# Kernel optimization log

Hardware: AMD Instinct MI355X
Metric: run time of the kernel (lower is better)

## Reference

```python
import jax, jax.numpy as jnp
import numpy as np
import math

HEAD_SIZE = 64

def setup_inputs() -> dict:
    key = jax.random.key(0)
    k0, k1, k2, k3 = jax.random.split(key, 4)
    B, T, E, H = 4, 4096, 1024, HEAD_SIZE
    return {
        "x": jax.random.normal(k0, (B, T, E), dtype=jnp.float32),
        "Wq": jax.random.normal(k1, (E, H), dtype=jnp.float32) * (1.0 / math.sqrt(E)),
        "Wk": jax.random.normal(k2, (E, H), dtype=jnp.float32) * (1.0 / math.sqrt(E)),
        "Wv": jax.random.normal(k3, (E, H), dtype=jnp.float32) * (1.0 / math.sqrt(E)),
    }

def reference(x, Wq, Wk, Wv):
    # Single-head attention; faithful to source: softmax FIRST, then divide by sqrt(head_size)
    T = x.shape[-2]
    q = x @ Wq  # [B,T,H]
    k = x @ Wk
    v = x @ Wv
    scores = jnp.einsum('bth,bsh->bts', q, k)  # [B,T,T]
    # 'encoder' mask in this repo = lower-triangular (causal)
    causal = jnp.tril(jnp.ones((T, T), dtype=bool))
    scores = jnp.where(causal, scores, -jnp.inf)
    attn = jax.nn.softmax(scores, axis=-1) / jnp.sqrt(jnp.float32(q.shape[-1]))
    return jnp.einsum('bts,bsh->bth', attn, v)
```

## Files before the change

kernel.cpp:

```cpp
#include <hip/hip_runtime.h>
#include <math.h>

#define BB 4
#define TT 4096
#define EE 1024
#define HH 64

typedef __attribute__((ext_vector_type(8))) short bf16x8;
typedef _Float16 f16x8 __attribute__((ext_vector_type(8)));
typedef __attribute__((ext_vector_type(4))) float f32x4;

#define MFMA16(a, b, c)  __builtin_amdgcn_mfma_f32_16x16x32_bf16(a, b, c, 0, 0, 0)
#define MFMA16F(a, b, c) __builtin_amdgcn_mfma_f32_16x16x32_f16(a, b, c, 0, 0, 0)

__device__ __forceinline__ unsigned short f2bf_rne(float f) {
    unsigned u = __float_as_uint(f);
    unsigned r = u + 0x7fffu + ((u >> 16) & 1u);
    return (unsigned short)(r >> 16);
}
__device__ __forceinline__ float bf2f(unsigned short h) {
    return __uint_as_float(((unsigned)h) << 16);
}
__device__ __forceinline__ unsigned short f2h(float f) {
    union { _Float16 h; unsigned short u; } cv;
    cv.h = (_Float16)f;
    return cv.u;
}

__device__ __forceinline__ void async_copy16(const void* g, void* l) {
    __builtin_amdgcn_global_load_lds(
        (const __attribute__((address_space(1))) void*)g,
        (__attribute__((address_space(3))) void*)l, 16, 0, 0);
}
template<int N>
__device__ __forceinline__ void wait_vm() {
    __builtin_amdgcn_s_waitcnt(0x0f70 | (N & 15) | ((N >> 4) << 14));
}

__global__ __launch_bounds__(256) void wprep_kernel(
    const float* __restrict__ Wq, const float* __restrict__ Wk,
    const float* __restrict__ Wv,
    unsigned short* __restrict__ wt)
{
    __shared__ float ts[64][65];
    const int which = blockIdx.x >> 4;
    const int e0 = (blockIdx.x & 15) * 64;
    const float* W = (which == 0) ? Wq : ((which == 1) ? Wk : Wv);
    const int t = threadIdx.x;
    const int h = t & 63;
    #pragma unroll
    for (int p = 0; p < 16; p++) {
        const int er = (t >> 6) + p * 4;
        ts[er][h] = W[(size_t)(e0 + er) * 64 + h];
    }
    __syncthreads();
    const int ew = t & 63;
    #pragma unroll
    for (int p = 0; p < 16; p++) {
        const int hh = (t >> 6) + p * 4;
        const float f = ts[ew][hh];
        const size_t o = (size_t)(which * 64 + hh) * 1024 + e0 + ew;
        wt[o] = f2h(f);
    }
}

__global__ __launch_bounds__(512) void proj_kernel(
    const float* __restrict__ x,
    const unsigned short* __restrict__ wt,
    unsigned short* __restrict__ qhf, unsigned short* __restrict__ qlf,
    unsigned short* __restrict__ kf, unsigned short* __restrict__ vt)
{
    __shared__ __align__(16) unsigned char smem[147456];
    const int tid = threadIdx.x;
    const int w = tid >> 6, lane = tid & 63;
    const int quad = lane >> 4, li = lane & 15;
    const int tg = w & 3, eh = w >> 2;
    const int row0 = (int)blockIdx.x * 64;
    const int tok = row0 + tg * 16 + li;

    f32x4 acc[12];
    #pragma unroll
    for (int mt = 0; mt < 12; mt++) acc[mt] = (f32x4){0.f, 0.f, 0.f, 0.f};

    const float* xr = x + (size_t)tok * EE + eh * 512 + quad * 8;

    const int r_l = lane >> 3, sl = lane & 7;
    const int c_l = sl ^ r_l;

    auto dma_step = [&](int e0, unsigned char* dstbase) {
        #pragma unroll
        for (int ii = 0; ii < 6; ii++) {
            const int i = w * 6 + ii;
            const int ehc = i / 24;
            const int within = i % 24;
            const int row = within * 8 + r_l;
            const unsigned short* src = wt + (size_t)row * EE + ehc * 512 + e0 + c_l * 8;
            async_copy16(src, dstbase + ehc * 24576 + within * 1024);
        }
    };

    const int r7 = li & 7;
    const int slot0 = ((0 + quad) ^ r7) * 8;
    const int slot1 = ((4 + quad) ^ r7) * 8;

    dma_step(0, smem);
    float4 fc0 = *(const float4*)(xr + 0);
    float4 fc1 = *(const float4*)(xr + 4);
    float4 fc2 = *(const float4*)(xr + 32);
    float4 fc3 = *(const float4*)(xr + 36);
    dma_step(64, smem + 49152);
    float4 fn0 = *(const float4*)(xr + 64);
    float4 fn1 = *(const float4*)(xr + 68);
    float4 fn2 = *(const float4*)(xr + 96);
    float4 fn3 = *(const float4*)(xr + 100);
    float4 ff0, ff1, ff2, ff3;

    for (int s = 0; s < 8; s++) {
        if (s + 2 < 8) {
            const int e2 = (s + 2) * 64;
            dma_step(e2, smem + ((s + 2) % 3) * 49152);
            ff0 = *(const float4*)(xr + e2);
            ff1 = *(const float4*)(xr + e2 + 4);
            ff2 = *(const float4*)(xr + e2 + 32);
            ff3 = *(const float4*)(xr + e2 + 36);
            wait_vm<20>();
        } else if (s + 1 < 8) {
            wait_vm<10>();
        } else {
            wait_vm<0>();
        }
        __builtin_amdgcn_s_barrier();

        const _Float16* Wbase = (const _Float16*)(smem + (s % 3) * 49152)
                                + eh * 12288 + (li >> 3) * 512 + r7 * 64;

        #pragma unroll
        for (int ks = 0; ks < 2; ks++) {
            const float4 va = ks ? fc2 : fc0;
            const float4 vb = ks ? fc3 : fc1;
            float fv[8] = {va.x, va.y, va.z, va.w, vb.x, vb.y, vb.z, vb.w};
            f16x8 bh, bl;
            #pragma unroll
            for (int jj = 0; jj < 8; jj++) {
                const _Float16 hh = (_Float16)fv[jj];
                bh[jj] = hh;
                bl[jj] = (_Float16)(fv[jj] - (float)hh);
            }
            const int slot = ks ? slot1 : slot0;
            #pragma unroll
            for (int mt = 0; mt < 12; mt++) {
                const f16x8 A = *(const f16x8*)(Wbase + mt * 1024 + slot);
                acc[mt] = MFMA16F(A, bh, acc[mt]);
                acc[mt] = MFMA16F(A, bl, acc[mt]);
            }
        }
        __builtin_amdgcn_s_barrier();
        fc0 = fn0; fc1 = fn1; fc2 = fn2; fc3 = fn3;
        fn0 = ff0; fn1 = ff1; fn2 = ff2; fn3 = ff3;
    }

    float* Red = (float*)smem;
    if (eh == 1) {
        #pragma unroll
        for (int mt = 0; mt < 12; mt++)
            #pragma unroll
            for (int r = 0; r < 4; r++)
                Red[(size_t)(tg * 192 + mt * 16 + quad * 4 + r) * 17 + li] = acc[mt][r];
    }
    __syncthreads();
    if (eh == 0) {
        #pragma unroll
        for (int mt = 0; mt < 12; mt++)
            #pragma unroll
            for (int r = 0; r < 4; r++)
                acc[mt][r] += Red[(size_t)(tg * 192 + mt * 16 + quad * 4 + r) * 17 + li];
        const int bb = tok >> 12, tloc = tok & 4095;
        #pragma unroll
        for (int mt = 0; mt < 12; mt++) {
            if (mt < 4) {
                const int h = (mt & 3) * 16 + quad * 4;
                ushort4 hi4, lo4; float f; _Float16 hh;
                union { _Float16 h; unsigned short u; } cv;
                f = acc[mt][0]; hh = (_Float16)f; cv.h = hh; hi4.x = cv.u; lo4.x = f2h(f - (float)hh);
                f = acc[mt][1]; hh = (_Float16)f; cv.h = hh; hi4.y = cv.u; lo4.y = f2h(f - (float)hh);
                f = acc[mt][2]; hh = (_Float16)f; cv.h = hh; hi4.z = cv.u; lo4.z = f2h(f - (float)hh);
                f = acc[mt][3]; hh = (_Float16)f; cv.h = hh; hi4.w = cv.u; lo4.w = f2h(f - (float)hh);
                const size_t o = (size_t)tok * 64 + h;
                *(ushort4*)(qhf + o) = hi4;
                *(ushort4*)(qlf + o) = lo4;
            } else if (mt < 8) {
                const int h = (mt & 3) * 16 + quad * 4;
                ushort4 k4;
                k4.x = f2h(acc[mt][0]); k4.y = f2h(acc[mt][1]);
                k4.z = f2h(acc[mt][2]); k4.w = f2h(acc[mt][3]);
                *(ushort4*)(kf + (size_t)tok * 64 + h) = k4;
            } else {
                const int hv = (mt - 8) * 16 + quad * 4;
                #pragma unroll
                for (int r = 0; r < 4; r++)
                    vt[((size_t)(bb * 64 + hv + r) << 12) + tloc] = f2bf_rne(acc[mt][r]);
            }
        }
    }
}

__global__ __launch_bounds__(512) void flash_kernel(
    const unsigned short* __restrict__ qhf, const unsigned short* __restrict__ qlf,
    const unsigned short* __restrict__ kf,
    const unsigned short* __restrict__ vt, float* __restrict__ out)
{
    __shared__ __align__(16) unsigned char smem[119808];
    const int tid = threadIdx.x;
    const int w = tid >> 6, lane = tid & 63;
    const int quad = lane >> 4, li = lane & 15;
    const int lb = (int)blockIdx.x;
    const int b  = (lb & 7) >> 1;
    const int bx = ((lb >> 3) << 1) | (lb & 1);
    const float SM = 20.0f;

    const _Float16* kb = (const _Float16*)kf + ((size_t)b << 18);
    const unsigned short* vtb = vt + ((size_t)b << 18) + (size_t)li * 4096 + quad * 8;

    unsigned char* kbase = smem + w * 12288;
    unsigned short* PsA = (unsigned short*)(smem + 98304 + w * 2560);
    unsigned short* PsB = PsA + 640;
    float* Op = (float*)smem;
    float* Ml = (float*)(smem + 118784);

    const int r_l8 = lane >> 3, s8 = lane & 7;
    const int slf0 = ((quad)     ^ (li & 7)) * 8;
    const int slf1 = ((4 + quad) ^ (li & 7)) * 8;

    auto dma_tile = [&](int k0, unsigned char* dst) {
        #pragma unroll
        for (int i = 0; i < 4; i++) {
            const int row = i * 8 + r_l8;
            const int c = s8 ^ r_l8;
            async_copy16(kb + (size_t)(k0 + row) * 64 + c * 8, dst + i * 1024);
        }
    };

    #pragma unroll 1
    for (int phase = 0; phase < 2; phase++) {
        const int g = phase ? (127 - bx) : bx;
        const int q0 = g * 32;
        const int n_kt = g + 1;
        const int tok0 = q0 + li, tok1 = tok0 + 16;

        const size_t qo0 = ((size_t)(b << 12) + tok0) * 64 + quad * 8;
        const size_t qo1 = qo0 + 16 * 64;
        const _Float16* qh_p = (const _Float16*)qhf;
        const _Float16* ql_p = (const _Float16*)qlf;
        const f16x8 QhA0 = *(const f16x8*)(qh_p + qo0);
        const f16x8 QhA1 = *(const f16x8*)(qh_p + qo0 + 32);
        const f16x8 QlA0 = *(const f16x8*)(ql_p + qo0);
        const f16x8 QlA1 = *(const f16x8*)(ql_p + qo0 + 32);
        const f16x8 QhB0 = *(const f16x8*)(qh_p + qo1);
        const f16x8 QhB1 = *(const f16x8*)(qh_p + qo1 + 32);
        const f16x8 QlB0 = *(const f16x8*)(ql_p + qo1);
        const f16x8 QlB1 = *(const f16x8*)(ql_p + qo1 + 32);

        f32x4 accA[4], accB[4];
        #pragma unroll
        for (int mt = 0; mt < 4; mt++) {
            accA[mt] = (f32x4){0.f, 0.f, 0.f, 0.f};
            accB[mt] = (f32x4){0.f, 0.f, 0.f, 0.f};
        }
        float lA = 0.f, lB = 0.f;

        bf16x8 Vc[4], Vn[4], Vm[4];
        if (w < n_kt) {
            dma_tile(w * 32, kbase);
            #pragma unroll
            for (int hf = 0; hf < 4; hf++)
                Vc[hf] = *(const bf16x8*)(vtb + (size_t)hf * 65536 + w * 32);
        }
        if (w + 8 < n_kt) {
            dma_tile((w + 8) * 32, kbase + 4096);
            #pragma unroll
            for (int hf = 0; hf < 4; hf++)
                Vn[hf] = *(const bf16x8*)(vtb + (size_t)hf * 65536 + (w + 8) * 32);
        }

        int n_it = 0;
        for (int kt = w; kt < n_kt; kt += 8, n_it++) {
            const int k0 = kt * 32;
            const int slot = n_it % 3;

            if (kt + 16 < n_kt) {
                const int s2p = slot + 2;
                const int slot2 = (s2p >= 3) ? s2p - 3 : s2p;
                dma_tile((kt + 16) * 32, kbase + slot2 * 4096);
                #pragma unroll
                for (int hf = 0; hf < 4; hf++)
                    Vm[hf] = *(const bf16x8*)(vtb + (size_t)hf * 65536 + (kt + 16) * 32);
                wait_vm<16>();
            } else if (kt + 8 < n_kt) {
                wait_vm<8>();
            } else {
                wait_vm<0>();
            }
            const _Float16* Kw = (const _Float16*)(kbase + slot * 4096);

            f32x4 sA[2], sB[2];
            #pragma unroll
            for (int jf = 0; jf < 2; jf++) {
                const _Float16* rb = Kw + (jf * 16 + li) * 64;
                f16x8 K0 = *(const f16x8*)(rb + slf0);
                f16x8 K1 = *(const f16x8*)(rb + slf1);
                f32x4 a = (f32x4){0.f, 0.f, 0.f, 0.f};
                a = MFMA16F(K0, QhA0, a);
                a = MFMA16F(K1, QhA1, a);
                a = MFMA16F(K0, QlA0, a);
                a = MFMA16F(K1, QlA1, a);
                sA[jf] = a;
                f32x4 c2 = (f32x4){0.f, 0.f, 0.f, 0.f};
                c2 = MFMA16F(K0, QhB0, c2);
                c2 = MFMA16F(K1, QhB1, c2);
                c2 = MFMA16F(K0, QlB0, c2);
                c2 = MFMA16F(K1, QlB1, c2);
                sB[jf] = c2;
            }

            if (kt == n_kt - 1) {
                #pragma unroll
                for (int jf = 0; jf < 2; jf++)
                    #pragma unroll
                    for (int r = 0; r < 4; r++) {
                        const int j = k0 + jf * 16 + quad * 4 + r;
                        if (j > tok0) sA[jf][r] = -1e30f;
                        if (j > tok1) sB[jf][r] = -1e30f;
                    }
            }

            #pragma unroll
            for (int jf = 0; jf < 2; jf++)
                #pragma unroll
                for (int r = 0; r < 4; r++) {
                    sA[jf][r] = __expf(sA[jf][r] - SM); lA += sA[jf][r];
                    sB[jf][r] = __expf(sB[jf][r] - SM); lB += sB[jf][r];
                }

            #pragma unroll
            for (int jf = 0; jf < 2; jf++) {
                ushort4 pa, pb;
                pa.x = f2bf_rne(sA[jf][0]); pa.y = f2bf_rne(sA[jf][1]);
                pa.z = f2bf_rne(sA[jf][2]); pa.w = f2bf_rne(sA[jf][3]);
                pb.x = f2bf_rne(sB[jf][0]); pb.y = f2bf_rne(sB[jf][1]);
                pb.z = f2bf_rne(sB[jf][2]); pb.w = f2bf_rne(sB[jf][3]);
                *(ushort4*)&PsA[li * 40 + jf * 16 + quad * 4] = pa;
                *(ushort4*)&PsB[li * 40 + jf * 16 + quad * 4] = pb;
            }
            const bf16x8 PA = *(const bf16x8*)&PsA[li * 40 + quad * 8];
            const bf16x8 PB = *(const bf16x8*)&PsB[li * 40 + quad * 8];

            #pragma unroll
            for (int hf = 0; hf < 4; hf++) {
                accA[hf] = MFMA16(Vc[hf], PA, accA[hf]);
                accB[hf] = MFMA16(Vc[hf], PB, accB[hf]);
            }
            #pragma unroll
            for (int hf = 0; hf < 4; hf++) { Vc[hf] = Vn[hf]; Vn[hf] = Vm[hf]; }
        }

        lA += __shfl_xor(lA, 16); lA += __shfl_xor(lA, 32);
        lB += __shfl_xor(lB, 16); lB += __shfl_xor(lB, 32);

        __syncthreads();
        #pragma unroll
        for (int mt = 0; mt < 4; mt++)
            #pragma unroll
            for (int r = 0; r < 4; r++) {
                Op[(size_t)w * 2112 + (mt * 16 + quad * 4 + r) * 33 + li]      = accA[mt][r];
                Op[(size_t)w * 2112 + (mt * 16 + quad * 4 + r) * 33 + li + 16] = accB[mt][r];
            }
        if (quad == 0) {
            Ml[w * 32 + li]      = lA;
            Ml[w * 32 + 16 + li] = lB;
        }
        __syncthreads();

        const int i  = tid >> 4;
        const int hc = (tid & 15) * 4;
        float l = 0.f;
        #pragma unroll
        for (int ww = 0; ww < 8; ww++) l += Ml[ww * 32 + i];
        const float inv = 1.0f / (l * 8.0f);
        float4 o = {0.f, 0.f, 0.f, 0.f};
        #pragma unroll
        for (int ww = 0; ww < 8; ww++) {
            const float* base = Op + (size_t)ww * 2112;
            o.x += base[(hc + 0) * 33 + i];
            o.y += base[(hc + 1) * 33 + i];
            o.z += base[(hc + 2) * 33 + i];
            o.w += base[(hc + 3) * 33 + i];
        }
        o.x *= inv; o.y *= inv; o.z *= inv; o.w *= inv;
        *(float4*)(out + ((size_t)(b << 12) + q0 + i) * 64 + hc) = o;
        __syncthreads();
    }
}

extern "C" void kernel_launch(void* const* d_in, const int* in_sizes, int n_in,
                              void* d_out, int out_size, void* d_ws, size_t ws_size,
                              hipStream_t stream)
{
    const float* x  = (const float*)d_in[0];
    const float* Wq = (const float*)d_in[1];
    const float* Wk = (const float*)d_in[2];
    const float* Wv = (const float*)d_in[3];
    float* out = (float*)d_out;

    const size_t n_tok = (size_t)BB * TT * HH;
    unsigned short* qhf = (unsigned short*)d_ws;
    unsigned short* qlf = qhf + n_tok;
    unsigned short* kf  = qlf + n_tok;
    unsigned short* vt  = kf + n_tok;
    unsigned short* wt  = vt + n_tok;

    wprep_kernel<<<48, 256, 0, stream>>>(Wq, Wk, Wv, wt);
    proj_kernel<<<(BB * TT) / 64, 512, 0, stream>>>(x, wt,
                                                    qhf, qlf, kf, vt);
    flash_kernel<<<256, 512, 0, stream>>>(qhf, qlf, kf, vt, out);
}
```

Measured before the change: 146.5 us.

## Process 128 tokens per projection block to reuse LDS weight tiles

Each projection block now handles two 16-token fragments per warp, 128 tokens in all. Each weight fragment read from LDS now feeds MFMAs for both fragments, with the x prefetch, wait counts, reduction and output stores extended to match. This halves the weight DMA and LDS traffic per token. In exchange the grid is halved to 128 blocks, which may leave many CUs idle, and accumulator and prefetch register pressure doubles.

Measured after the change: 159.7 us. +9.0%, slower.

```diff
diff --git a/kernel.cpp b/kernel.cpp
--- a/kernel.cpp
+++ b/kernel.cpp
@@ -75,14 +75,18 @@
     const int w = tid >> 6, lane = tid & 63;
     const int quad = lane >> 4, li = lane & 15;
     const int tg = w & 3, eh = w >> 2;
-    const int row0 = (int)blockIdx.x * 64;
-    const int tok = row0 + tg * 16 + li;
-
-    f32x4 acc[12];
+    const int row0 = (int)blockIdx.x * 128;
+    const int tokA = row0 + tg * 32 + li;
+
+    f32x4 acc[12][2];
     #pragma unroll
-    for (int mt = 0; mt < 12; mt++) acc[mt] = (f32x4){0.f, 0.f, 0.f, 0.f};
-
-    const float* xr = x + (size_t)tok * EE + eh * 512 + quad * 8;
+    for (int mt = 0; mt < 12; mt++) {
+        acc[mt][0] = (f32x4){0.f, 0.f, 0.f, 0.f};
+        acc[mt][1] = (f32x4){0.f, 0.f, 0.f, 0.f};
+    }
+
+    const float* xrA = x + (size_t)tokA * EE + eh * 512 + quad * 8;
+    const float* xrB = xrA + (size_t)16 * EE;
 
     const int r_l = lane >> 3, sl = lane & 7;
     const int c_l = sl ^ r_l;
@@ -98,34 +102,35 @@
             async_copy16(src, dstbase + ehc * 24576 + within * 1024);
         }
     };
+    auto load_x = [&](int e0, float4* d) {
+        d[0] = *(const float4*)(xrA + e0);
+        d[1] = *(const float4*)(xrA + e0 + 4);
+        d[2] = *(const float4*)(xrA + e0 + 32);
+        d[3] = *(const float4*)(xrA + e0 + 36);
+        d[4] = *(const float4*)(xrB + e0);
+        d[5] = *(const float4*)(xrB + e0 + 4);
+        d[6] = *(const float4*)(xrB + e0 + 32);
+        d[7] = *(const float4*)(xrB + e0 + 36);
+    };
 
     const int r7 = li & 7;
     const int slot0 = ((0 + quad) ^ r7) * 8;
     const int slot1 = ((4 + quad) ^ r7) * 8;
 
+    float4 fc[8], fn[8], ff[8];
     dma_step(0, smem);
-    float4 fc0 = *(const float4*)(xr + 0);
-    float4 fc1 = *(const float4*)(xr + 4);
-    float4 fc2 = *(const float4*)(xr + 32);
-    float4 fc3 = *(const float4*)(xr + 36);
+    load_x(0, fc);
     dma_step(64, smem + 49152);
-    float4 fn0 = *(const float4*)(xr + 64);
-    float4 fn1 = *(const float4*)(xr + 68);
-    float4 fn2 = *(const float4*)(xr + 96);
-    float4 fn3 = *(const float4*)(xr + 100);
-    float4 ff0, ff1, ff2, ff3;
+    load_x(64, fn);
 
     for (int s = 0; s < 8; s++) {
         if (s + 2 < 8) {
             const int e2 = (s + 2) * 64;
             dma_step(e2, smem + ((s + 2) % 3) * 49152);
-            ff0 = *(const float4*)(xr + e2);
-            ff1 = *(const float4*)(xr + e2 + 4);
-            ff2 = *(const float4*)(xr + e2 + 32);
-            ff3 = *(const float4*)(xr + e2 + 36);
-            wait_vm<20>();
+            load_x(e2, ff);
+            wait_vm<28>();
         } else if (s + 1 < 8) {
-            wait_vm<10>();
+            wait_vm<14>();
         } else {
             wait_vm<0>();
         }
@@ -136,69 +141,83 @@
 
         #pragma unroll
         for (int ks = 0; ks < 2; ks++) {
-            const float4 va = ks ? fc2 : fc0;
-            const float4 vb = ks ? fc3 : fc1;
-            float fv[8] = {va.x, va.y, va.z, va.w, vb.x, vb.y, vb.z, vb.w};
-            f16x8 bh, bl;
+            const float4 va = fc[ks * 2 + 0], vb = fc[ks * 2 + 1];
+            float fvA[8] = {va.x, va.y, va.z, va.w, vb.x, vb.y, vb.z, vb.w};
+            const float4 vc = fc[ks * 2 + 4], vd = fc[ks * 2 + 5];
+            float fvB[8] = {vc.x, vc.y, vc.z, vc.w, vd.x, vd.y, vd.z, vd.w};
+            f16x8 bhA, blA, bhB, blB;
             #pragma unroll
             for (int jj = 0; jj < 8; jj++) {
-                const _Float16 hh = (_Float16)fv[jj];
-                bh[jj] = hh;
-                bl[jj] = (_Float16)(fv[jj] - (float)hh);
+                _Float16 hh = (_Float16)fvA[jj];
+                bhA[jj] = hh;
+                blA[jj] = (_Float16)(fvA[jj] - (float)hh);
+                hh = (_Float16)fvB[jj];
+                bhB[jj] = hh;
+                blB[jj] = (_Float16)(fvB[jj] - (float)hh);
             }
             const int slot = ks ? slot1 : slot0;
             #pragma unroll
             for (int mt = 0; mt < 12; mt++) {
                 const f16x8 A = *(const f16x8*)(Wbase + mt * 1024 + slot);
-                acc[mt] = MFMA16F(A, bh, acc[mt]);
-                acc[mt] = MFMA16F(A, bl, acc[mt]);
+                acc[mt][0] = MFMA16F(A, bhA, acc[mt][0]);
+                acc[mt][0] = MFMA16F(A, blA, acc[mt][0]);
+                acc[mt][1] = MFMA16F(A, bhB, acc[mt][1]);
+                acc[mt][1] = MFMA16F(A, blB, acc[mt][1]);
             }
         }
         __builtin_amdgcn_s_barrier();
-        fc0 = fn0; fc1 = fn1; fc2 = fn2; fc3 = fn3;
-        fn0 = ff0; fn1 = ff1; fn2 = ff2; fn3 = ff3;
+        #pragma unroll
+        for (int j = 0; j < 8; j++) { fc[j] = fn[j]; fn[j] = ff[j]; }
     }
 
     float* Red = (float*)smem;
     if (eh == 1) {
         #pragma unroll
-        for (int mt = 0; mt < 12; mt++)
-            #pragma unroll
-            for (int r = 0; r < 4; r++)
-                Red[(size_t)(tg * 192 + mt * 16 + quad * 4 + r) * 17 + li] = acc[mt][r];
+        for (int f = 0; f < 2; f++)
+            #pragma unroll
+            for (int mt = 0; mt < 12; mt++)
+                #pragma unroll
+                for (int r = 0; r < 4; r++)
+                    Red[(size_t)((tg * 2 + f) * 192 + mt * 16 + quad * 4 + r) * 17 + li]
+                        = acc[mt][f][r];
     }
     __syncthreads();
     if (eh == 0) {
         #pragma unroll
-        for (int mt = 0; mt < 12; mt++)
-            #pragma unroll
-            for (int r = 0; r < 4; r++)
-                acc[mt][r] += Red[(size_t)(tg * 192 + mt * 16 + quad * 4 + r) * 17 + li];
-        const int bb = tok >> 12, tloc = tok & 4095;
-        #pragma unroll
-        for (int mt = 0; mt < 12; mt++) {
-            if (mt < 4) {
-                const int h = (mt & 3) * 16 + quad * 4;
-                ushort4 hi4, lo4; float f; _Float16 hh;
-                union { _Float16 h; unsigned short u; } cv;
-                f = acc[mt][0]; hh = (_Float16)f; cv.h = hh; hi4.x = cv.u; lo4.x = f2h(f - (float)hh);
-                f = acc[mt][1]; hh = (_Float16)f; cv.h = hh; hi4.y = cv.u; lo4.y = f2h(f - (float)hh);
-                f = acc[mt][2]; hh = (_Float16)f; cv.h = hh; hi4.z = cv.u; lo4.z = f2h(f - (float)hh);
-                f = acc[mt][3]; hh = (_Float16)f; cv.h = hh; hi4.w = cv.u; lo4.w = f2h(f - (float)hh);
-                const size_t o = (size_t)tok * 64 + h;
-                *(ushort4*)(qhf + o) = hi4;
-                *(ushort4*)(qlf + o) = lo4;
-            } else if (mt < 8) {
-                const int h = (mt & 3) * 16 + quad * 4;
-                ushort4 k4;
-                k4.x = f2h(acc[mt][0]); k4.y = f2h(acc[mt][1]);
-                k4.z = f2h(acc[mt][2]); k4.w = f2h(acc[mt][3]);
-                *(ushort4*)(kf + (size_t)tok * 64 + h) = k4;
-            } else {
-                const int hv = (mt - 8) * 16 + quad * 4;
+        for (int f = 0; f < 2; f++) {
+            #pragma unroll
+            for (int mt = 0; mt < 12; mt++)
                 #pragma unroll
                 for (int r = 0; r < 4; r++)
-                    vt[((size_t)(bb * 64 + hv + r) << 12) + tloc] = f2bf_rne(acc[mt][r]);
+                    acc[mt][f][r] +=
+                        Red[(size_t)((tg * 2 + f) * 192 + mt * 16 + quad * 4 + r) * 17 + li];
+            const int tok = tokA + f * 16;
+            const int bb = tok >> 12, tloc = tok & 4095;
+            #pragma unroll
+            for (int mt = 0; mt < 12; mt++) {
+                if (mt < 4) {
+                    const int h = (mt & 3) * 16 + quad * 4;
+                    ushort4 hi4, lo4; float fl; _Float16 hh;
+                    union { _Float16 h; unsigned short u; } cv;
+                    fl = acc[mt][f][0]; hh = (_Float16)fl; cv.h = hh; hi4.x = cv.u; lo4.x = f2h(fl - (float)hh);
+                    fl = acc[mt][f][1]; hh = (_Float16)fl; cv.h = hh; hi4.y = cv.u; lo4.y = f2h(fl - (float)hh);
+                    fl = acc[mt][f][2]; hh = (_Float16)fl; cv.h = hh; hi4.z = cv.u; lo4.z = f2h(fl - (float)hh);
+                    fl = acc[mt][f][3]; hh = (_Float16)fl; cv.h = hh; hi4.w = cv.u; lo4.w = f2h(fl - (float)hh);
+                    const size_t o = (size_t)tok * 64 + h;
+                    *(ushort4*)(qhf + o) = hi4;
+                    *(ushort4*)(qlf + o) = lo4;
+                } else if (mt < 8) {
+                    const int h = (mt & 3) * 16 + quad * 4;
+                    ushort4 k4;
+                    k4.x = f2h(acc[mt][f][0]); k4.y = f2h(acc[mt][f][1]);
+                    k4.z = f2h(acc[mt][f][2]); k4.w = f2h(acc[mt][f][3]);
+                    *(ushort4*)(kf + (size_t)tok * 64 + h) = k4;
+                } else {
+                    const int hv = (mt - 8) * 16 + quad * 4;
+                    #pragma unroll
+                    for (int r = 0; r < 4; r++)
+                        vt[((size_t)(bb * 64 + hv + r) << 12) + tloc] = f2bf_rne(acc[mt][f][r]);
+                }
             }
         }
     }
@@ -419,7 +438,7 @@
     unsigned short* wt  = vt + n_tok;
 
     wprep_kernel<<<48, 256, 0, stream>>>(Wq, Wk, Wv, wt);
-    proj_kernel<<<(BB * TT) / 64, 512, 0, stream>>>(x, wt,
-                                                    qhf, qlf, kf, vt);
+    proj_kernel<<<(BB * TT) / 128, 512, 0, stream>>>(x, wt,
+                                                     qhf, qlf, kf, vt);
     flash_kernel<<<256, 512, 0, stream>>>(qhf, qlf, kf, vt, out);
 }
```
